# Kernel tuning notes

Measured on AMD Instinct MI355X. Metric: run time of the kernel, lower is better.

The kernel has to match this reference:

```python
import jax, jax.numpy as jnp
import numpy as np

DT = 0.02          # full control timestep (cfg dt)
N_SUBSTEPS = 8     # RK4 substeps per forward call
LMBDA = 0.5        # first-order actuator lag gain
G_VEC = jnp.array([0.0, 0.0, -9.81], dtype=jnp.float32)
N_ENVS = 2097152


def setup_inputs() -> dict:
    key = jax.random.key(0)
    k1, k2 = jax.random.split(key)
    X0 = jax.random.normal(k1, (N_ENVS, 9), dtype=jnp.float32)
    U = jax.random.normal(k2, (N_ENVS, 3), dtype=jnp.float32)
    return {"X0": X0, "U": U}


def reference(X0, U):
    h = DT / N_SUBSTEPS  # substep size

    def dynamics(X):
        v = X[:, 3:6]
        a = X[:, 6:9]
        a_dot = LMBDA * (U - a) / DT   # actuator lag uses full dt, as in torch code
        # X_dot = [p_dot, v_dot, a_dot] = [v, a - g_vec, a_dot]
        return jnp.concatenate([v, a - G_VEC, a_dot], axis=-1)

    def rk4_step(X, _):
        k1 = dynamics(X)
        k2 = dynamics(X + 0.5 * h * k1)
        k3 = dynamics(X + 0.5 * h * k2)
        k4 = dynamics(X + h * k3)
        X_next = X + (h / 6.0) * (k1 + 2.0 * k2 + 2.0 * k3 + k4)
        return X_next, None

    X_final, _ = jax.lax.scan(rk4_step, X0, None, length=N_SUBSTEPS)
    return X_final
```

## Files before the change

### kernel.cpp

```cpp
#include <hip/hip_runtime.h>


#define ENVS_PER_BLOCK 1024
#define THREADS 256
#define XF4 (ENVS_PER_BLOCK * 9 / 4)
#define UF4 (ENVS_PER_BLOCK * 3 / 4)

typedef float f32x4 __attribute__((ext_vector_type(4)));

__device__ __forceinline__ f32x4 nt_load4(const float* p) {
    return __builtin_nontemporal_load((const f32x4*)p);
}
__device__ __forceinline__ void nt_store4(float* p, const f32x4 v) {
    __builtin_nontemporal_store(v, (f32x4*)p);
}

struct Coeffs {
    float P00, P01, P02;
    float P10, P11, P12;
    float P20, P21, P22;
    float Ku0, Ku1, Ku2;
    float Kg0, Kg1, Kg2;
};

__device__ __forceinline__ void compute_env(const float* __restrict__ sx,
                                            const float* __restrict__ su,
                                            const Coeffs& cf, float r[9]) {
    #pragma unroll
    for (int k = 0; k < 3; ++k) {
        const float p = sx[k];
        const float v = sx[3 + k];
        const float a = sx[6 + k];
        const float u = su[k];
        const float g = (k == 2) ? -9.81f : 0.0f;
        r[k]     = cf.P00 * p + cf.P01 * v + cf.P02 * a + cf.Ku0 * u + cf.Kg0 * g;
        r[3 + k] = cf.P10 * p + cf.P11 * v + cf.P12 * a + cf.Ku1 * u + cf.Kg1 * g;
        r[6 + k] = cf.P20 * p + cf.P21 * v + cf.P22 * a + cf.Ku2 * u + cf.Kg2 * g;
    }
}

__global__ __launch_bounds__(THREADS)
void pointmass_kernel(const float* __restrict__ X0,
                      const float* __restrict__ U,
                      float* __restrict__ Out,
                      int envTotal, Coeffs cf) {
    __shared__ float s_x[ENVS_PER_BLOCK * 9];
    __shared__ float s_u[ENVS_PER_BLOCK * 3];

    const int t = threadIdx.x;
    const int blockBase = blockIdx.x * ENVS_PER_BLOCK;
    const int envsHere = min(ENVS_PER_BLOCK, envTotal - blockBase);

    if (envsHere == ENVS_PER_BLOCK) {
        const float* xg = X0 + (size_t)blockBase * 9;
        const float* ug = U  + (size_t)blockBase * 3;
        float* og = Out + (size_t)blockBase * 9;

        f32x4 xr[9], ur[3];
        #pragma unroll
        for (int q = 0; q < 9; ++q) xr[q] = nt_load4(xg + (q * THREADS + t) * 4);
        #pragma unroll
        for (int q = 0; q < 3; ++q) ur[q] = nt_load4(ug + (q * THREADS + t) * 4);
        #pragma unroll
        for (int q = 0; q < 9; ++q) ((f32x4*)s_x)[q * THREADS + t] = xr[q];
        #pragma unroll
        for (int q = 0; q < 3; ++q) ((f32x4*)s_u)[q * THREADS + t] = ur[q];
        __syncthreads();

        #pragma unroll
        for (int ee = 0; ee < 4; ++ee) {
            const int e = t + ee * THREADS;
            float r[9];
            compute_env(s_x + e * 9, s_u + e * 3, cf, r);
            #pragma unroll
            for (int i = 0; i < 9; ++i) s_x[e * 9 + i] = r[i];
        }
        __syncthreads();

        #pragma unroll
        for (int q = 0; q < 9; ++q) {
            const f32x4 v = ((const f32x4*)s_x)[q * THREADS + t];
            nt_store4(og + (q * THREADS + t) * 4, v);
        }
    } else {
        for (int j = t; j < envsHere * 9; j += THREADS)
            s_x[j] = X0[(size_t)blockBase * 9 + j];
        for (int j = t; j < envsHere * 3; j += THREADS)
            s_u[j] = U[(size_t)blockBase * 3 + j];
        __syncthreads();
        for (int e = t; e < envsHere; e += THREADS) {
            float r[9];
            compute_env(s_x + e * 9, s_u + e * 3, cf, r);
            #pragma unroll
            for (int i = 0; i < 9; ++i)
                Out[((size_t)blockBase + e) * 9 + i] = r[i];
        }
    }
}

static void mat3_mul(const double A[3][3], const double B[3][3], double C[3][3]) {
    for (int i = 0; i < 3; ++i)
        for (int j = 0; j < 3; ++j) {
            double s = 0.0;
            for (int k = 0; k < 3; ++k) s += A[i][k] * B[k][j];
            C[i][j] = s;
        }
}
static void mat3_copy(const double A[3][3], double B[3][3]) {
    for (int i = 0; i < 3; ++i) for (int j = 0; j < 3; ++j) B[i][j] = A[i][j];
}

extern "C" void kernel_launch(void* const* d_in, const int* in_sizes, int n_in,
                              void* d_out, int out_size, void* d_ws, size_t ws_size,
                              hipStream_t stream) {
    const float* X0 = (const float*)d_in[0];
    const float* U  = (const float*)d_in[1];
    float* Out = (float*)d_out;
    const int envTotal = in_sizes[0] / 9;

    const double DT = 0.02;
    const double h = DT / 8.0;
    const double c = 0.5 / DT;
    double hA[3][3] = {{0, h, 0}, {0, 0, h}, {0, 0, -c * h}};

    double hA2[3][3], hA3[3][3], hA4[3][3];
    mat3_mul(hA, hA, hA2);
    mat3_mul(hA2, hA, hA3);
    mat3_mul(hA3, hA, hA4);

    double P[3][3], Q[3][3];
    for (int i = 0; i < 3; ++i)
        for (int j = 0; j < 3; ++j) {
            const double I = (i == j) ? 1.0 : 0.0;
            P[i][j] = I + hA[i][j] + hA2[i][j] / 2.0 + hA3[i][j] / 6.0 + hA4[i][j] / 24.0;
            Q[i][j] = h * (I + hA[i][j] / 2.0 + hA2[i][j] / 6.0 + hA3[i][j] / 24.0);
        }

    double P2[3][3], P4[3][3], P8[3][3];
    mat3_mul(P, P, P2);
    mat3_mul(P2, P2, P4);
    mat3_mul(P4, P4, P8);

    double IP[3][3], IP2[3][3], IP4[3][3], T[3][3], S[3][3], R[3][3];
    mat3_copy(P, IP);  mat3_copy(P2, IP2);  mat3_copy(P4, IP4);
    for (int i = 0; i < 3; ++i) { IP[i][i] += 1.0; IP2[i][i] += 1.0; IP4[i][i] += 1.0; }
    mat3_mul(IP, IP2, T);
    mat3_mul(T, IP4, S);
    mat3_mul(S, Q, R);

    Coeffs cf;
    cf.P00 = (float)P8[0][0]; cf.P01 = (float)P8[0][1]; cf.P02 = (float)P8[0][2];
    cf.P10 = (float)P8[1][0]; cf.P11 = (float)P8[1][1]; cf.P12 = (float)P8[1][2];
    cf.P20 = (float)P8[2][0]; cf.P21 = (float)P8[2][1]; cf.P22 = (float)P8[2][2];
    cf.Ku0 = (float)(R[0][2] * c); cf.Ku1 = (float)(R[1][2] * c); cf.Ku2 = (float)(R[2][2] * c);
    cf.Kg0 = (float)(-R[0][1]);    cf.Kg1 = (float)(-R[1][1]);    cf.Kg2 = (float)(-R[2][1]);

    const int blocks = (envTotal + ENVS_PER_BLOCK - 1) / ENVS_PER_BLOCK;
    pointmass_kernel<<<blocks, THREADS, 0, stream>>>(X0, U, Out, envTotal, cf);
}
```

Before: 145.6 us.

## Replace shared-memory staging with per-thread contiguous 4-env register loads

Each thread now loads the 144 contiguous bytes for four envs straight into registers with nine 16-byte vector loads (plus three for U), computes, and writes back directly. This removes the shared-memory staging, both block barriers and the LDS traffic. The catch is that neighbouring lanes now access addresses 144 bytes apart, so each load instruction is strided rather than fully coalesced, which relies on the cache to merge requests. Register pressure also rises.

```diff
diff --git a/kernel.cpp b/kernel.cpp
--- a/kernel.cpp
+++ b/kernel.cpp
@@ -1,10 +1,7 @@
 #include <hip/hip_runtime.h>
 
 
-#define ENVS_PER_BLOCK 1024
 #define THREADS 256
-#define XF4 (ENVS_PER_BLOCK * 9 / 4)
-#define UF4 (ENVS_PER_BLOCK * 3 / 4)
 
 typedef float f32x4 __attribute__((ext_vector_type(4)));
 
@@ -23,19 +20,18 @@
     float Kg0, Kg1, Kg2;
 };
 
-__device__ __forceinline__ void compute_env(const float* __restrict__ sx,
-                                            const float* __restrict__ su,
-                                            const Coeffs& cf, float r[9]) {
+__device__ __forceinline__ void compute9(const float x[9], const float u[3],
+                                         const Coeffs& cf, float r[9]) {
     #pragma unroll
     for (int k = 0; k < 3; ++k) {
-        const float p = sx[k];
-        const float v = sx[3 + k];
-        const float a = sx[6 + k];
-        const float u = su[k];
+        const float p = x[k];
+        const float v = x[3 + k];
+        const float a = x[6 + k];
+        const float uu = u[k];
         const float g = (k == 2) ? -9.81f : 0.0f;
-        r[k]     = cf.P00 * p + cf.P01 * v + cf.P02 * a + cf.Ku0 * u + cf.Kg0 * g;
-        r[3 + k] = cf.P10 * p + cf.P11 * v + cf.P12 * a + cf.Ku1 * u + cf.Kg1 * g;
-        r[6 + k] = cf.P20 * p + cf.P21 * v + cf.P22 * a + cf.Ku2 * u + cf.Kg2 * g;
+        r[k]     = cf.P00 * p + cf.P01 * v + cf.P02 * a + cf.Ku0 * uu + cf.Kg0 * g;
+        r[3 + k] = cf.P10 * p + cf.P11 * v + cf.P12 * a + cf.Ku1 * uu + cf.Kg1 * g;
+        r[6 + k] = cf.P20 * p + cf.P21 * v + cf.P22 * a + cf.Ku2 * uu + cf.Kg2 * g;
     }
 }
 
@@ -44,56 +40,54 @@
                       const float* __restrict__ U,
                       float* __restrict__ Out,
                       int envTotal, Coeffs cf) {
-    __shared__ float s_x[ENVS_PER_BLOCK * 9];
-    __shared__ float s_u[ENVS_PER_BLOCK * 3];
+    const int g4 = blockIdx.x * THREADS + threadIdx.x;
+    const size_t e0 = (size_t)g4 * 4;
 
-    const int t = threadIdx.x;
-    const int blockBase = blockIdx.x * ENVS_PER_BLOCK;
-    const int envsHere = min(ENVS_PER_BLOCK, envTotal - blockBase);
+    if (e0 + 4 <= (size_t)envTotal) {
+        const float* xp = X0 + e0 * 9;
+        const float* up = U  + e0 * 3;
+        float* op = Out + e0 * 9;
 
-    if (envsHere == ENVS_PER_BLOCK) {
-        const float* xg = X0 + (size_t)blockBase * 9;
-        const float* ug = U  + (size_t)blockBase * 3;
-        float* og = Out + (size_t)blockBase * 9;
+        f32x4 xv[9], uv[3];
+        #pragma unroll
+        for (int q = 0; q < 9; ++q) xv[q] = nt_load4(xp + 4 * q);
+        #pragma unroll
+        for (int q = 0; q < 3; ++q) uv[q] = nt_load4(up + 4 * q);
 
-        f32x4 xr[9], ur[3];
+        float xs[36], us[12];
         #pragma unroll
-        for (int q = 0; q < 9; ++q) xr[q] = nt_load4(xg + (q * THREADS + t) * 4);
+        for (int q = 0; q < 9; ++q) {
+            #pragma unroll
+            for (int j = 0; j < 4; ++j) xs[4 * q + j] = xv[q][j];
+        }
         #pragma unroll
-        for (int q = 0; q < 3; ++q) ur[q] = nt_load4(ug + (q * THREADS + t) * 4);
+        for (int q = 0; q < 3; ++q) {
+            #pragma unroll
+            for (int j = 0; j < 4; ++j) us[4 * q + j] = uv[q][j];
+        }
+
+        float os[36];
         #pragma unroll
-        for (int q = 0; q < 9; ++q) ((f32x4*)s_x)[q * THREADS + t] = xr[q];
-        #pragma unroll
-        for (int q = 0; q < 3; ++q) ((f32x4*)s_u)[q * THREADS + t] = ur[q];
-        __syncthreads();
-
-        #pragma unroll
-        for (int ee = 0; ee < 4; ++ee) {
-            const int e = t + ee * THREADS;
-            float r[9];
-            compute_env(s_x + e * 9, s_u + e * 3, cf, r);
-            #pragma unroll
-            for (int i = 0; i < 9; ++i) s_x[e * 9 + i] = r[i];
-        }
-        __syncthreads();
+        for (int e = 0; e < 4; ++e)
+            compute9(xs + 9 * e, us + 3 * e, cf, os + 9 * e);
 
         #pragma unroll
         for (int q = 0; q < 9; ++q) {
-            const f32x4 v = ((const f32x4*)s_x)[q * THREADS + t];
-            nt_store4(og + (q * THREADS + t) * 4, v);
+            f32x4 v;
+            #pragma unroll
+            for (int j = 0; j < 4; ++j) v[j] = os[4 * q + j];
+            nt_store4(op + 4 * q, v);
         }
-    } else {
-        for (int j = t; j < envsHere * 9; j += THREADS)
-            s_x[j] = X0[(size_t)blockBase * 9 + j];
-        for (int j = t; j < envsHere * 3; j += THREADS)
-            s_u[j] = U[(size_t)blockBase * 3 + j];
-        __syncthreads();
-        for (int e = t; e < envsHere; e += THREADS) {
-            float r[9];
-            compute_env(s_x + e * 9, s_u + e * 3, cf, r);
+    } else if (e0 < (size_t)envTotal) {
+        for (size_t e = e0; e < (size_t)envTotal; ++e) {
+            float x[9], u[3], r[9];
             #pragma unroll
-            for (int i = 0; i < 9; ++i)
-                Out[((size_t)blockBase + e) * 9 + i] = r[i];
+            for (int q = 0; q < 9; ++q) x[q] = X0[e * 9 + q];
+            #pragma unroll
+            for (int k = 0; k < 3; ++k) u[k] = U[e * 3 + k];
+            compute9(x, u, cf, r);
+            #pragma unroll
+            for (int q = 0; q < 9; ++q) Out[e * 9 + q] = r[q];
         }
     }
 }
@@ -155,6 +149,7 @@
     cf.Ku0 = (float)(R[0][2] * c); cf.Ku1 = (float)(R[1][2] * c); cf.Ku2 = (float)(R[2][2] * c);
     cf.Kg0 = (float)(-R[0][1]);    cf.Kg1 = (float)(-R[1][1]);    cf.Kg2 = (float)(-R[2][1]);
 
-    const int blocks = (envTotal + ENVS_PER_BLOCK - 1) / ENVS_PER_BLOCK;
+    const int groups = (envTotal + 3) / 4;
+    const int blocks = (groups + THREADS - 1) / THREADS;
     pointmass_kernel<<<blocks, THREADS, 0, stream>>>(X0, U, Out, envTotal, cf);
 }
```

After: 225.4 us. +54.8%, slower.
